# Performance work log

Hardware: AMD Instinct MI355X
Metric: run time of the kernel (lower is better)

## Reference

```python
import jax, jax.numpy as jnp
import numpy as np

MAX_VARS = 10
EMBED_DIM = 128
PATCH = (16, 16)


def setup_inputs() -> dict:
    key = jax.random.key(0)
    k1, k2, k3, k4 = jax.random.split(key, 4)
    x = jax.random.normal(k1, (16, 8, 512, 512), dtype=jnp.float32)
    in_vars = jax.random.randint(k2, (8,), 0, MAX_VARS, dtype=jnp.int64)
    proj_weights = jax.random.normal(k3, (MAX_VARS, EMBED_DIM, 1, PATCH[0], PATCH[1]), dtype=jnp.float32)
    proj_biases = jax.random.normal(k4, (MAX_VARS, EMBED_DIM), dtype=jnp.float32)
    return {"x": x, "in_vars": in_vars, "proj_weights": proj_weights, "proj_biases": proj_biases}


def reference(x, in_vars, proj_weights, proj_biases):
    # x: [B, V, H, W]; proj_weights: [max_vars, E, 1, ph, pw]
    B, V, H, W = x.shape
    E, ph, pw = proj_weights.shape[1], proj_weights.shape[3], proj_weights.shape[4]
    gh, gw = H // ph, W // pw
    w = proj_weights[in_vars, :, 0]       # [V, E, ph, pw] gathered per-variable weights
    b = proj_biases[in_vars]              # [V, E]
    # kernel==stride grouped conv == non-overlapping patchify + per-variable matmul
    xp = x.reshape(B, V, gh, ph, gw, pw)
    out = jnp.einsum('bvhpwq,vepq->bvhwe', xp, w)  # [B, V, gh, gw, E]
    out = out.reshape(B, V, gh * gw, E) + b[None, :, None, :]
    return out  # [B, V, num_patches, E]
```

## Files before the change

### kernel.cpp

```cpp
#include <hip/hip_runtime.h>

#define NB 16
#define NV 8
#define HW 512
#define PH 16
#define GH 32
#define ED 128
#define KD 256
#define MAXV 10

#define LDS_STRIDE 264

typedef __bf16 bf16x8 __attribute__((ext_vector_type(8)));
typedef __bf16 bf16x4 __attribute__((ext_vector_type(4)));
typedef float  f32x4  __attribute__((ext_vector_type(4)));

__global__ __launch_bounds__(256) void pack_weights(const float* __restrict__ w,
                                                    __bf16* __restrict__ packed) {
    int tid = blockIdx.x * 256 + threadIdx.x;
    if (tid >= MAXV * ED * KD) return;
    int t   = tid & 31;
    int n   = (tid >> 5) & 127;
    int kb  = (tid >> 12) & 7;
    int var = tid >> 15;
    int k   = kb * 32 + t;
    float f = w[(var * ED + n) * KD + k];
    packed[tid] = (__bf16)f;
}

__global__ __launch_bounds__(256) void patch_embed(
    const float* __restrict__ x,
    const int*   __restrict__ in_vars,
    const __bf16* __restrict__ wpacked,
    const float* __restrict__ bias,
    float* __restrict__ out)
{
    __shared__ __bf16 As[32 * LDS_STRIDE];

    const int bx  = blockIdx.x;
    const int h   = bx & 31;
    const int v   = (bx >> 5) & 7;
    const int b   = bx >> 8;
    const int tid = threadIdx.x;

    const int var = in_vars[v];

    const float* xb = x + (((size_t)(b * NV + v)) * HW + (size_t)h * PH) * HW;

    #pragma unroll
    for (int i = 0; i < 8; ++i) {
        int idx = tid + i * 256;
        int p   = idx >> 7;
        int c   = (idx & 127) << 2;
        float4 f = *(const float4*)(xb + (size_t)p * HW + c);
        int m = c >> 4;
        int q = c & 15;
        bf16x4 bv;
        bv.x = (__bf16)f.x; bv.y = (__bf16)f.y; bv.z = (__bf16)f.z; bv.w = (__bf16)f.w;
        *(bf16x4*)&As[m * LDS_STRIDE + p * PH + q] = bv;
    }
    __syncthreads();

    const int wave  = tid >> 6;
    const int lane  = tid & 63;
    const int lo    = lane & 15;
    const int quad  = lane >> 4;
    const int nwave = wave * 32;

    const __bf16* wbase = wpacked + (size_t)var * (ED * KD);

    f32x4 acc[2][2];
    #pragma unroll
    for (int i = 0; i < 2; ++i)
        #pragma unroll
        for (int j = 0; j < 2; ++j)
            acc[i][j] = (f32x4){0.f, 0.f, 0.f, 0.f};

    #pragma unroll
    for (int kb = 0; kb < 8; ++kb) {
        bf16x8 aF[2], bF[2];
        #pragma unroll
        for (int i = 0; i < 2; ++i) {
            aF[i] = *(const bf16x8*)&As[(i * 16 + lo) * LDS_STRIDE + kb * 32 + quad * 8];
        }
        #pragma unroll
        for (int j = 0; j < 2; ++j) {
            bF[j] = *(const bf16x8*)&wbase[kb * 4096 + (nwave + j * 16 + lo) * 32 + quad * 8];
        }
        #pragma unroll
        for (int i = 0; i < 2; ++i)
            #pragma unroll
            for (int j = 0; j < 2; ++j)
                acc[i][j] = __builtin_amdgcn_mfma_f32_16x16x32_bf16(aF[i], bF[j], acc[i][j], 0, 0, 0);
    }

    float bv[2];
    #pragma unroll
    for (int j = 0; j < 2; ++j)
        bv[j] = bias[var * ED + nwave + j * 16 + lo];

    const size_t outbase = ((size_t)(b * NV + v)) * (GH * GH) + (size_t)h * GH;
    #pragma unroll
    for (int i = 0; i < 2; ++i) {
        #pragma unroll
        for (int r = 0; r < 4; ++r) {
            int m = i * 16 + quad * 4 + r;
            #pragma unroll
            for (int j = 0; j < 2; ++j) {
                int e = nwave + j * 16 + lo;
                out[(outbase + m) * ED + e] = acc[i][j][r] + bv[j];
            }
        }
    }
}

extern "C" void kernel_launch(void* const* d_in, const int* in_sizes, int n_in,
                              void* d_out, int out_size, void* d_ws, size_t ws_size,
                              hipStream_t stream) {
    const float* x       = (const float*)d_in[0];
    const int*   in_vars = (const int*)d_in[1];
    const float* w       = (const float*)d_in[2];
    const float* bias    = (const float*)d_in[3];
    float*       out     = (float*)d_out;
    __bf16*      wpacked = (__bf16*)d_ws;

    hipLaunchKernelGGL(pack_weights, dim3((MAXV * ED * KD + 255) / 256), dim3(256), 0, stream,
                       w, wpacked);
    hipLaunchKernelGGL(patch_embed, dim3(NB * NV * GH), dim3(256), 0, stream,
                       x, in_vars, wpacked, bias, out);
}
```

Measured before the change: 220.0 us.

## Load A fragments directly from global memory, dropping LDS staging and barrier

Removes the shared-memory tile for input patches. Each wave now reads its MFMA A fragments straight from global memory and converts them to bf16 in registers. All weight fragments are preloaded into registers before the loop, and the launch bounds request higher occupancy. This avoids LDS writes, reads and a block barrier, but every wave redundantly fetches the same input rows, relying on caches to absorb the duplication.

Result: slower. 238.3 us (+8.3%).

```diff
diff --git a/kernel.cpp b/kernel.cpp
--- a/kernel.cpp
+++ b/kernel.cpp
@@ -9,10 +9,7 @@
 #define KD 256
 #define MAXV 10
 
-#define LDS_STRIDE 264
-
 typedef __bf16 bf16x8 __attribute__((ext_vector_type(8)));
-typedef __bf16 bf16x4 __attribute__((ext_vector_type(4)));
 typedef float  f32x4  __attribute__((ext_vector_type(4)));
 
 __global__ __launch_bounds__(256) void pack_weights(const float* __restrict__ w,
@@ -28,46 +25,36 @@
     packed[tid] = (__bf16)f;
 }
 
-__global__ __launch_bounds__(256) void patch_embed(
+__global__ __launch_bounds__(256, 4) void patch_embed(
     const float* __restrict__ x,
     const int*   __restrict__ in_vars,
     const __bf16* __restrict__ wpacked,
     const float* __restrict__ bias,
     float* __restrict__ out)
 {
-    __shared__ __bf16 As[32 * LDS_STRIDE];
-
     const int bx  = blockIdx.x;
     const int h   = bx & 31;
     const int v   = (bx >> 5) & 7;
     const int b   = bx >> 8;
     const int tid = threadIdx.x;
 
+    const int wave = tid >> 6;
+    const int lane = tid & 63;
+    const int lo   = lane & 15;
+    const int quad = lane >> 4;
+    const int nwave = wave * 32;
+
     const int var = in_vars[v];
 
     const float* xb = x + (((size_t)(b * NV + v)) * HW + (size_t)h * PH) * HW;
+    const __bf16* wbase = wpacked + (size_t)var * (ED * KD);
 
+    bf16x8 bF[8][2];
     #pragma unroll
-    for (int i = 0; i < 8; ++i) {
-        int idx = tid + i * 256;
-        int p   = idx >> 7;
-        int c   = (idx & 127) << 2;
-        float4 f = *(const float4*)(xb + (size_t)p * HW + c);
-        int m = c >> 4;
-        int q = c & 15;
-        bf16x4 bv;
-        bv.x = (__bf16)f.x; bv.y = (__bf16)f.y; bv.z = (__bf16)f.z; bv.w = (__bf16)f.w;
-        *(bf16x4*)&As[m * LDS_STRIDE + p * PH + q] = bv;
-    }
-    __syncthreads();
-
-    const int wave  = tid >> 6;
-    const int lane  = tid & 63;
-    const int lo    = lane & 15;
-    const int quad  = lane >> 4;
-    const int nwave = wave * 32;
-
-    const __bf16* wbase = wpacked + (size_t)var * (ED * KD);
+    for (int kb = 0; kb < 8; ++kb)
+        #pragma unroll
+        for (int j = 0; j < 2; ++j)
+            bF[kb][j] = *(const bf16x8*)&wbase[kb * 4096 + (nwave + j * 16 + lo) * 32 + quad * 8];
 
     f32x4 acc[2][2];
     #pragma unroll
@@ -76,22 +63,26 @@
         for (int j = 0; j < 2; ++j)
             acc[i][j] = (f32x4){0.f, 0.f, 0.f, 0.f};
 
+    const float* abase = xb + (size_t)(quad >> 1) * HW + lo * PH + (quad & 1) * 8;
+
     #pragma unroll
     for (int kb = 0; kb < 8; ++kb) {
-        bf16x8 aF[2], bF[2];
+        bf16x8 aF[2];
         #pragma unroll
         for (int i = 0; i < 2; ++i) {
-            aF[i] = *(const bf16x8*)&As[(i * 16 + lo) * LDS_STRIDE + kb * 32 + quad * 8];
-        }
-        #pragma unroll
-        for (int j = 0; j < 2; ++j) {
-            bF[j] = *(const bf16x8*)&wbase[kb * 4096 + (nwave + j * 16 + lo) * 32 + quad * 8];
+            const float* pA = abase + (size_t)(2 * kb) * HW + i * 256;
+            float4 f0 = *(const float4*)pA;
+            float4 f1 = *(const float4*)(pA + 4);
+            bf16x8 t;
+            t[0] = (__bf16)f0.x; t[1] = (__bf16)f0.y; t[2] = (__bf16)f0.z; t[3] = (__bf16)f0.w;
+            t[4] = (__bf16)f1.x; t[5] = (__bf16)f1.y; t[6] = (__bf16)f1.z; t[7] = (__bf16)f1.w;
+            aF[i] = t;
         }
         #pragma unroll
         for (int i = 0; i < 2; ++i)
             #pragma unroll
             for (int j = 0; j < 2; ++j)
-                acc[i][j] = __builtin_amdgcn_mfma_f32_16x16x32_bf16(aF[i], bF[j], acc[i][j], 0, 0, 0);
+                acc[i][j] = __builtin_amdgcn_mfma_f32_16x16x32_bf16(aF[i], bF[kb][j], acc[i][j], 0, 0, 0);
     }
 
     float bv[2];
```
